# Kernel tuning notes

Measured on AMD Instinct MI355X. Metric: run time of the kernel, lower is better.

The kernel has to match this reference:

```python
import jax, jax.numpy as jnp
import numpy as np

SHIFT, REDUCE = 0, 1
B, T, E, H = 128, 256, 300, 256


def _make_transitions(T, B):
    # Valid left-branching sequence: S, S, (R, S)*, ending with R -> 2T-1 steps.
    t = np.zeros(2 * T - 1, dtype=np.int32)
    t[2::2] = REDUCE
    return np.tile(t[:, None], (1, B))


def setup_inputs() -> dict:
    key = jax.random.key(0)
    ks = jax.random.split(key, 8)
    stdv = 1.0 / np.sqrt(H)
    u = lambda k, shape: jax.random.uniform(k, shape, jnp.float32, -stdv, stdv)
    return {
        "x": jax.random.normal(ks[0], (B, T, E), jnp.float32),
        "transitions": jnp.asarray(_make_transitions(T, B)),
        "Wp": u(ks[1], (E, H)),
        "bp": u(ks[2], (H,)),
        "Wg": u(ks[3], (E, H)),
        "bg": u(ks[4], (H,)),
        "Wr": u(ks[5], (2 * H, 5 * H)),
        "br": u(ks[6], (5 * H,)),
    }


def reference(x, transitions, Wp, bp, Wg, bg, Wr, br):
    Bb, Tt, _ = x.shape
    Hh = Wp.shape[1]
    # buffers: c = proj_x(x); h = sigmoid(proj_x_gate(x)) * tanh(c)
    c_buf = x @ Wp + bp                      # [B, T, H]
    h_buf = jax.nn.sigmoid(x @ Wg + bg) * jnp.tanh(c_buf)
    bidx = jnp.arange(Bb)

    stack_h0 = jnp.zeros((Bb, Tt, Hh), x.dtype)
    stack_c0 = jnp.zeros((Bb, Tt, Hh), x.dtype)
    sp0 = jnp.zeros((Bb,), jnp.int32)        # stack pointer
    bp0 = jnp.full((Bb,), Tt, jnp.int32)     # buffer pointer (pop from end)

    def step(carry, trans):
        sh, sc, sp, bptr = carry
        is_shift = trans == SHIFT            # [B] bool
        # SHIFT: pop last remaining buffer entry
        nbp = jnp.where(is_shift, bptr - 1, bptr)
        src = jnp.maximum(nbp, 0)
        sft_h = h_buf[bidx, src]
        sft_c = c_buf[bidx, src]
        # REDUCE: children = top two stack entries (r = top, l = below)
        ir = jnp.maximum(sp - 1, 0)
        il = jnp.maximum(sp - 2, 0)
        hl, cl = sh[bidx, il], sc[bidx, il]
        hr, cr = sh[bidx, ir], sc[bidx, ir]
        proj = jnp.concatenate([hl, hr], axis=-1) @ Wr + br   # [B, 5H]
        i, fl, fr, g, o = jnp.split(proj, 5, axis=-1)
        c_red = (jax.nn.sigmoid(fl) * cl + jax.nn.sigmoid(fr) * cr
                 + jax.nn.sigmoid(i) * jnp.tanh(g))
        h_red = jax.nn.sigmoid(o) * jnp.tanh(c_red)
        m = is_shift[:, None]
        h_new = jnp.where(m, sft_h, h_red)
        c_new = jnp.where(m, sft_c, c_red)
        pos = jnp.where(is_shift, sp, il)    # push location
        sh = sh.at[bidx, pos].set(h_new)
        sc = sc.at[bidx, pos].set(c_new)
        sp = jnp.where(is_shift, sp + 1, sp - 1)
        return (sh, sc, sp, nbp), None

    (sh, sc, sp, _), _ = jax.lax.scan(step, (stack_h0, stack_c0, sp0, bp0), transitions)
    # root h state = top of stack, h half only
    return sh[bidx, jnp.maximum(sp - 1, 0)]
```

## Files before the change

kernel.cpp:

```cpp
#include <hip/hip_runtime.h>
#include <hip/hip_fp16.h>
#include <math.h>

#define B_ 128
#define T_ 256
#define E_ 300
#define H_ 256
#define N5_ 1280
#define NSTEPS 511
#define DMAX 8

typedef _Float16 half8_t __attribute__((ext_vector_type(8)));
typedef float float4_t __attribute__((ext_vector_type(4)));
typedef unsigned int u4v __attribute__((ext_vector_type(4)));

__device__ __forceinline__ float sigm_p(float x){ return 1.f/(1.f + expf(-x)); }
__device__ __forceinline__ float sigm(float x){ return __builtin_amdgcn_rcpf(1.f + __expf(-x)); }
__device__ __forceinline__ float ftanh(float x){
  float xc = fminf(15.f, fmaxf(-15.f, x));
  float e = __expf(-2.f*xc);
  return (1.f - e) * __builtin_amdgcn_rcpf(1.f + e);
}

__device__ __forceinline__ int dot4(int a, int b, int c){
#if __has_builtin(__builtin_amdgcn_sdot4)
  return __builtin_amdgcn_sdot4(a, b, c, false);
#else
  int d;
  asm("v_dot4_i32_i8 %0, %1, %2, %3" : "=v"(d) : "v"(a), "v"(b), "v"(c));
  return d;
#endif
}

__global__ __launch_bounds__(64) void k0a_scale(const float* __restrict__ Wr,
    float* __restrict__ scales){
  const int n = blockIdx.x, t = threadIdx.x;
  float m = 0.f;
  #pragma unroll
  for (int j=0;j<4;j++) m = fmaxf(m, fabsf(Wr[(size_t)(t+64*j)*N5_ + n]));
  #pragma unroll
  for (int off=32; off; off>>=1) m = fmaxf(m, __shfl_xor(m, off, 64));
  if (t==0) scales[n] = fmaxf(m, 1e-20f) * (1.f/127.f);
}

__global__ __launch_bounds__(256) void k0b_quant(const float* __restrict__ Wr,
    const float* __restrict__ scales, unsigned* __restrict__ W8){
  int idx = blockIdx.x*256 + threadIdx.x;
  if (idx >= 81920) return;
  const int col = idx >> 6, kd = idx & 63;
  const float inv = 1.f / scales[col];
  unsigned acc = 0;
  #pragma unroll
  for (int j=0;j<4;j++){
    float wv = Wr[(size_t)(4*kd + j)*N5_ + col];
    int q = (int)rintf(wv * inv);
    q = q > 127 ? 127 : (q < -127 ? -127 : q);
    acc |= ((unsigned)(q & 255)) << (8*j);
  }
  W8[idx] = acc;
}

__global__ __launch_bounds__(256) void k1_proj(
    const float* __restrict__ x, const float* __restrict__ Wp, const float* __restrict__ bp,
    const float* __restrict__ Wg, const float* __restrict__ bg,
    _Float16* __restrict__ h2, _Float16* __restrict__ c2){
  __shared__ __align__(16) _Float16 As [64*32];
  __shared__ __align__(16) _Float16 BsP[64*32];
  __shared__ __align__(16) _Float16 BsG[64*32];
  const int tid = threadIdx.x;
  const int row0 = blockIdx.x * 64;
  const int n0   = blockIdx.y * 64;
  const int wave = tid >> 6, lane = tid & 63;
  const int ml = lane & 15, quad = lane >> 4;
  float4_t accP[4], accG[4];
  #pragma unroll
  for (int i=0;i<4;i++){ accP[i]=(float4_t)(0.f); accG[i]=(float4_t)(0.f); }
  const int ar = tid >> 2, ak = (tid & 3) * 8;
  const int bk = tid >> 3, bn = (tid & 7) * 8;
  for (int kk = 0; kk < E_; kk += 32){
    __syncthreads();
    {
      const float* src = x + (size_t)(row0 + ar)*E_ + kk + ak;
      float v[8];
      #pragma unroll
      for (int q=0;q<2;q++){
        if (kk + ak + q*4 + 4 <= E_){
          float4_t f = *(const float4_t*)(src + q*4);
          v[q*4+0]=f.x; v[q*4+1]=f.y; v[q*4+2]=f.z; v[q*4+3]=f.w;
        } else {
          #pragma unroll
          for (int j=0;j<4;j++){ int kg = kk+ak+q*4+j; v[q*4+j] = (kg<E_) ? src[q*4+j] : 0.f; }
        }
      }
      #pragma unroll
      for (int j=0;j<8;j++) As[ar*32 + ak + j] = (_Float16)v[j];
    }
    {
      const int kg = kk + bk;
      if (kg < E_){
        const float* sp_ = Wp + (size_t)kg*H_ + n0 + bn;
        const float* sg_ = Wg + (size_t)kg*H_ + n0 + bn;
        float4_t p0 = *(const float4_t*)sp_, p1 = *(const float4_t*)(sp_+4);
        float4_t g0 = *(const float4_t*)sg_, g1 = *(const float4_t*)(sg_+4);
        float pv[8]={p0.x,p0.y,p0.z,p0.w,p1.x,p1.y,p1.z,p1.w};
        float gv[8]={g0.x,g0.y,g0.z,g0.w,g1.x,g1.y,g1.z,g1.w};
        #pragma unroll
        for (int j=0;j<8;j++){ BsP[(bn+j)*32+bk]=(_Float16)pv[j]; BsG[(bn+j)*32+bk]=(_Float16)gv[j]; }
      } else {
        #pragma unroll
        for (int j=0;j<8;j++){ BsP[(bn+j)*32+bk]=(_Float16)0.f; BsG[(bn+j)*32+bk]=(_Float16)0.f; }
      }
    }
    __syncthreads();
    half8_t a = *(const half8_t*)&As[(wave*16 + ml)*32 + quad*8];
    #pragma unroll
    for (int nt=0; nt<4; nt++){
      half8_t b1 = *(const half8_t*)&BsP[(nt*16 + ml)*32 + quad*8];
      accP[nt] = __builtin_amdgcn_mfma_f32_16x16x32_f16(a, b1, accP[nt], 0,0,0);
      half8_t b2 = *(const half8_t*)&BsG[(nt*16 + ml)*32 + quad*8];
      accG[nt] = __builtin_amdgcn_mfma_f32_16x16x32_f16(a, b2, accG[nt], 0,0,0);
    }
  }
  #pragma unroll
  for (int nt=0; nt<4; nt++){
    #pragma unroll
    for (int r=0;r<4;r++){
      int row = row0 + wave*16 + quad*4 + r;
      int col = n0 + nt*16 + ml;
      float c = accP[nt][r] + bp[col];
      float g = accG[nt][r] + bg[col];
      float h = sigm_p(g) * tanhf(c);
      size_t o = (size_t)row*H_ + col;
      c2[o] = (_Float16)c;
      h2[o] = (_Float16)h;
    }
  }
}

__global__ __launch_bounds__(256) void k2_rproj(
    const _Float16* __restrict__ h2, const float* __restrict__ Wr, const float* __restrict__ br,
    _Float16* __restrict__ R2){
  __shared__ __align__(16) _Float16 As[64*32];
  __shared__ __align__(16) _Float16 Bs[64*32];
  const int tid = threadIdx.x;
  const int row0 = blockIdx.x*64, n0 = blockIdx.y*64;
  const int wave = tid>>6, lane = tid&63, ml = lane&15, quad = lane>>4;
  float4_t acc[4];
  #pragma unroll
  for (int i=0;i<4;i++) acc[i]=(float4_t)(0.f);
  const int ar = tid>>2, ak = (tid&3)*8;
  const int bk = tid>>3, bn = (tid&7)*8;
  for (int kk=0; kk<H_; kk+=32){
    __syncthreads();
    *(half8_t*)&As[ar*32+ak] = *(const half8_t*)(h2 + (size_t)(row0+ar)*H_ + kk + ak);
    {
      const float* src = Wr + (size_t)(256 + kk + bk)*N5_ + n0 + bn;
      float4_t f0 = *(const float4_t*)src, f1 = *(const float4_t*)(src+4);
      float v[8]={f0.x,f0.y,f0.z,f0.w,f1.x,f1.y,f1.z,f1.w};
      #pragma unroll
      for (int j=0;j<8;j++) Bs[(bn+j)*32+bk] = (_Float16)v[j];
    }
    __syncthreads();
    half8_t a = *(const half8_t*)&As[(wave*16+ml)*32 + quad*8];
    #pragma unroll
    for (int nt=0; nt<4; nt++){
      half8_t b8 = *(const half8_t*)&Bs[(nt*16+ml)*32 + quad*8];
      acc[nt] = __builtin_amdgcn_mfma_f32_16x16x32_f16(a, b8, acc[nt], 0,0,0);
    }
  }
  #pragma unroll
  for (int nt=0; nt<4; nt++){
    #pragma unroll
    for (int r=0;r<4;r++){
      int row = row0 + wave*16 + quad*4 + r;
      int col = n0 + nt*16 + ml;
      R2[(size_t)row*N5_ + col] = (_Float16)(acc[nt][r] + br[col]);
    }
  }
}

#define BARRIER() asm volatile("s_waitcnt lgkmcnt(0)\n\ts_barrier" ::: "memory")

#define DOT_ALL() \
  _Pragma("unroll") \
  for (int t=0; t<8; t++){ \
    _Pragma("unroll") \
    for (int j=0; j<4; j++){ \
      const int a = (int)aw[t][j]; \
      e0 = dot4(a, (int)wqv[   t][j], e0); \
      e1 = dot4(a, (int)wqv[ 8+t][j], e1); \
      e2 = dot4(a, (int)wqv[16+t][j], e2); \
      e3 = dot4(a, (int)wqv[24+t][j], e3); \
      e4 = dot4(a, (int)wqv[32+t][j], e4); \
    } \
  }

#define COMBINE_HALVES() \
  e0 += __shfl_xor(e0, 32, 64); \
  e1 += __shfl_xor(e1, 32, 64); \
  e2 += __shfl_xor(e2, 32, 64); \
  e3 += __shfl_xor(e3, 32, 64); \
  e4 += __shfl_xor(e4, 32, 64);

#define PAIR_STEP(IDX, RD, WR) { \
  BARRIER(); \
  float a0=(float)pA0, a1=(float)pA1, a2=(float)pA2, a3=(float)pA3, a4=(float)pA4; \
  const float tc = (float)pAc; \
  const u4v* sRD = (const u4v*)(sI8 + (RD)*H_); \
  u4v aw[8]; \
  _Pragma("unroll") \
  for (int t=0; t<8; t++) aw[t] = sRD[hh*8 + t]; \
  { int rrow = 253-(IDX); if (rrow < 0) rrow = 0; \
    const _Float16* rr = R2 + ((size_t)b*T_ + rrow)*N5_ + m; \
    pA0=rr[0]; pA1=rr[256]; pA2=rr[512]; pA3=rr[768]; pA4=rr[1024]; \
    int crow = 252-(IDX); if (crow < 0) crow = 0; \
    pAc = c2[((size_t)b*T_ + crow)*H_ + m]; } \
  int e0=0,e1=0,e2=0,e3=0,e4=0; \
  DOT_ALL() \
  COMBINE_HALVES() \
  a0 += scf0*(float)e0; a1 += scf1*(float)e1; a2 += scf2*(float)e2; \
  a3 += scf3*(float)e3; a4 += scf4*(float)e4; \
  const float cnew = sigm(a1)*cl + sigm(a2)*cr + sigm(a0)*ftanh(a3); \
  const float hnew = sigm(a4)*ftanh(cnew); \
  if (hh == 0) sI8[(WR)*H_ + m] = (char)(int)rintf(hnew*127.f); \
  cl = cnew; cr = tc; \
}

__global__ __launch_bounds__(512, 2) void k3_scan(
    const int* __restrict__ trans, const _Float16* __restrict__ h2, const _Float16* __restrict__ c2,
    const _Float16* __restrict__ R2, const unsigned* __restrict__ W8,
    const float* __restrict__ scales, const float* __restrict__ Wr,
    const float* __restrict__ br, float* __restrict__ out){
  __shared__ float sh_[DMAX*H_];
  __shared__ float sc_[DMAX*H_];
  __shared__ __align__(16) char sI8[DMAX*H_];
  __shared__ int trs[NSTEPS+1];

  const int b = blockIdx.x, tid = threadIdx.x;
  const int lane = tid & 63, w8 = tid >> 6;
  const int m  = w8*32 + (lane & 31);
  const int hh = (lane >> 5) & 1;

  u4v wqv[40];
  #pragma unroll
  for (int g=0; g<5; g++){
    const u4v* src = (const u4v*)(W8 + (size_t)(g*256 + m)*64 + hh*32);
    #pragma unroll
    for (int t=0; t<8; t++) wqv[g*8 + t] = src[t];
  }

  const float scf0 = scales[m       ] * (1.f/127.f);
  const float scf1 = scales[m +  256] * (1.f/127.f);
  const float scf2 = scales[m +  512] * (1.f/127.f);
  const float scf3 = scales[m +  768] * (1.f/127.f);
  const float scf4 = scales[m + 1024] * (1.f/127.f);

  trs[tid] = (tid < NSTEPS) ? trans[(size_t)tid*B_ + b] : 1;
  for (int i = tid; i < DMAX*H_; i += 512){ sh_[i]=0.f; sc_[i]=0.f; sI8[i]=0; }

  int myok = 1;
  if (tid < NSTEPS){ int e = (tid>=2 && (tid&1)==0) ? 1 : 0; if (trs[tid]!=e) myok=0; }
  const int ok = __syncthreads_and(myok);

  if (ok){
    const size_t hb = (size_t)b*T_*H_;
    const _Float16 h255 = h2[hb + 255*H_ + m];
    float cl = (float)c2[hb + 255*H_ + m];
    float cr = (float)c2[hb + 254*H_ + m];
    _Float16 pA0,pA1,pA2,pA3,pA4,pAc;
    { const _Float16* rr = R2 + ((size_t)b*T_ + 254)*N5_ + m;
      pA0=rr[0]; pA1=rr[256]; pA2=rr[512]; pA3=rr[768]; pA4=rr[1024];
      pAc = c2[hb + 253*H_ + m]; }
    if (hh == 0) sI8[m] = (char)(int)rintf((float)h255 * 127.f);
    #pragma unroll 1
    for (int i=0; i<254; i+=2){
      PAIR_STEP(i,   0, 1)
      PAIR_STEP(i+1, 1, 0)
    }
    {
      BARRIER();
      float a0=(float)pA0, a1=(float)pA1, a2=(float)pA2, a3=(float)pA3, a4=(float)pA4;
      const u4v* sRD = (const u4v*)sI8;
      u4v aw[8];
      #pragma unroll
      for (int t=0; t<8; t++) aw[t] = sRD[hh*8 + t];
      int e0=0,e1=0,e2=0,e3=0,e4=0;
      DOT_ALL()
      COMBINE_HALVES()
      a0 += scf0*(float)e0; a1 += scf1*(float)e1; a2 += scf2*(float)e2;
      a3 += scf3*(float)e3; a4 += scf4*(float)e4;
      const float cnew = sigm(a1)*cl + sigm(a2)*cr + sigm(a0)*ftanh(a3);
      const float hnew = sigm(a4)*ftanh(cnew);
      if (hh == 0) out[(size_t)b*H_ + m] = hnew;
    }
    return;
  }

  int sp = 0, bptr = T_, prev_src = -1;
  for (int step=0; step<NSTEPS; step++){
    __syncthreads();
    const int tr = trs[step];
    if (tr == 0){
      const int nbp = bptr - 1;
      const int src = nbp > 0 ? nbp : 0;
      const int slot = sp < 0 ? 0 : (sp > DMAX-1 ? DMAX-1 : sp);
      const size_t o = ((size_t)b*T_ + src)*H_ + m;
      const float wh = (float)h2[o], wc = (float)c2[o];
      if (hh == 0){
        sh_[slot*H_+m] = wh;
        sc_[slot*H_+m] = wc;
        sI8[slot*H_+m] = (char)(int)rintf(wh * 127.f);
      }
      sp += 1; bptr = nbp; prev_src = src;
    } else {
      int ir = sp-1 > 0 ? sp-1 : 0;
      int il = sp-2 > 0 ? sp-2 : 0;
      ir = ir > DMAX-1 ? DMAX-1 : ir;
      il = il > DMAX-1 ? DMAX-1 : il;
      const int tg = prev_src;
      const float cl = sc_[il*H_+m];
      const float cr = sc_[ir*H_+m];
      const u4v* sRD = (const u4v*)(sI8 + il*H_);
      u4v aw[8];
      #pragma unroll
      for (int t=0; t<8; t++) aw[t] = sRD[hh*8 + t];
      float a0,a1,a2,a3,a4;
      if (tg >= 0){
        const _Float16* rr = R2 + ((size_t)b*T_ + tg)*N5_ + m;
        a0=(float)rr[0]; a1=(float)rr[256]; a2=(float)rr[512]; a3=(float)rr[768]; a4=(float)rr[1024];
      } else {
        a0=br[m]; a1=br[m+256]; a2=br[m+512]; a3=br[m+768]; a4=br[m+1024];
      }
      int e0=0,e1=0,e2=0,e3=0,e4=0;
      DOT_ALL()
      COMBINE_HALVES()
      a0 += scf0*(float)e0; a1 += scf1*(float)e1; a2 += scf2*(float)e2;
      a3 += scf3*(float)e3; a4 += scf4*(float)e4;
      if (tg < 0){
        for (int k=0; k<H_; k++){
          const float hrk = sh_[ir*H_+k];
          const float* wr = Wr + (size_t)(256+k)*N5_ + m;
          a0 += hrk*wr[0]; a1 += hrk*wr[256]; a2 += hrk*wr[512];
          a3 += hrk*wr[768]; a4 += hrk*wr[1024];
        }
      }
      const float cnew = sigm(a1)*cl + sigm(a2)*cr + sigm(a0)*ftanh(a3);
      const float hnew = sigm(a4)*ftanh(cnew);
      const int wq = (int)rintf(hnew * 127.f);
      __syncthreads();
      if (hh == 0){
        sh_[il*H_+m] = hnew;
        sc_[il*H_+m] = cnew;
        sI8[il*H_+m] = (char)wq;
      }
      sp -= 1; prev_src = -1;
    }
  }
  __syncthreads();
  int fs = sp-1 > 0 ? sp-1 : 0;
  fs = fs > DMAX-1 ? DMAX-1 : fs;
  if (hh == 0) out[(size_t)b*H_ + m] = sh_[fs*H_+m];
}

extern "C" void kernel_launch(void* const* d_in, const int* in_sizes, int n_in,
                              void* d_out, int out_size, void* d_ws, size_t ws_size,
                              hipStream_t stream){
  const float* x    = (const float*)d_in[0];
  const int*   trn  = (const int*)  d_in[1];
  const float* Wp   = (const float*)d_in[2];
  const float* bp   = (const float*)d_in[3];
  const float* Wg   = (const float*)d_in[4];
  const float* bg   = (const float*)d_in[5];
  const float* Wr   = (const float*)d_in[6];
  const float* br   = (const float*)d_in[7];
  float* out = (float*)d_out;
  char* w = (char*)d_ws;
  _Float16* h2   = (_Float16*)(w);
  _Float16* c2   = (_Float16*)(w + (size_t)16777216);
  _Float16* R2   = (_Float16*)(w + (size_t)33554432);
  unsigned* W8   = (unsigned*)(w + (size_t)117440512);
  float*    scl  = (float*)   (w + (size_t)117768192);

  hipLaunchKernelGGL(k0a_scale, dim3(1280),    dim3(64),  0, stream, Wr, scl);
  hipLaunchKernelGGL(k0b_quant, dim3(320),     dim3(256), 0, stream, Wr, scl, W8);
  hipLaunchKernelGGL(k1_proj,   dim3(512, 4),  dim3(256), 0, stream, x, Wp, bp, Wg, bg, h2, c2);
  hipLaunchKernelGGL(k2_rproj,  dim3(512, 20), dim3(256), 0, stream, h2, Wr, br, R2);
  hipLaunchKernelGGL(k3_scan,   dim3(128),     dim3(512), 0, stream, trn, h2, c2, R2, W8, scl, Wr, br, out);
}
```

Measured before the change: 543.6 us.

## Move three gate matvecs in scan to int8 MFMA with AGPR-resident weights

In the recurrent scan, three of the five gate projections move from per-lane v_dot4 loops to v_mfma_i32_16x16x64_i8 chains. The weights for these are repacked into MFMA B-fragment layout by a new quantization kernel and kept in AGPRs. The remaining two gates keep dot4 and now reduce halves with permlane32_swap. The goal is to shorten the serial per-step compute latency and ease VGPR pressure. The cost is explicit s_nop fencing, an extra prep kernel, and wasted MFMA columns, since the matvec has only one useful row.

```diff
diff --git a/kernel.cpp b/kernel.cpp
--- a/kernel.cpp
+++ b/kernel.cpp
@@ -12,6 +12,7 @@
 
 typedef _Float16 half8_t __attribute__((ext_vector_type(8)));
 typedef float float4_t __attribute__((ext_vector_type(4)));
+typedef int i4v __attribute__((ext_vector_type(4)));
 typedef unsigned int u4v __attribute__((ext_vector_type(4)));
 
 __device__ __forceinline__ float sigm_p(float x){ return 1.f/(1.f + expf(-x)); }
@@ -32,6 +33,16 @@
 #endif
 }
 
+__device__ __forceinline__ int sum_halves(int e){
+#if __has_builtin(__builtin_amdgcn_permlane32_swap)
+  typedef unsigned u2v __attribute__((ext_vector_type(2)));
+  u2v r = __builtin_amdgcn_permlane32_swap((unsigned)e, (unsigned)e, false, false);
+  return (int)r[0] + (int)r[1];
+#else
+  return e + __shfl_xor(e, 32, 64);
+#endif
+}
+
 __global__ __launch_bounds__(64) void k0a_scale(const float* __restrict__ Wr,
     float* __restrict__ scales){
   const int n = blockIdx.x, t = threadIdx.x;
@@ -58,6 +69,38 @@
     acc |= ((unsigned)(q & 255)) << (8*j);
   }
   W8[idx] = acc;
+}
+
+__global__ __launch_bounds__(256) void k0c_quant(const float* __restrict__ Wr,
+    const float* __restrict__ scales, uint4* __restrict__ W4){
+  int idx = blockIdx.x*256 + threadIdx.x;
+  if (idx >= 20480) return;
+  const int f    = idx >> 6;
+  const int lane = idx & 63;
+  const int w    = f / 80;
+  const int r80  = f - w*80;
+  const int g    = r80 >> 4;
+  const int cg   = (r80 >> 2) & 3;
+  const int kc   = r80 & 3;
+  const int ml   = lane & 15, quad = lane >> 4;
+  const int col  = g*256 + w*64 + cg*16 + ml;
+  const float inv = 1.f / scales[col];
+  unsigned int d[4];
+  #pragma unroll
+  for (int r=0; r<4; r++){
+    unsigned int acc = 0;
+    #pragma unroll
+    for (int j=0; j<4; j++){
+      const int k = kc*64 + quad*16 + r*4 + j;
+      float wv = Wr[(size_t)k*N5_ + col];
+      int q = (int)rintf(wv * inv);
+      q = q > 127 ? 127 : (q < -127 ? -127 : q);
+      acc |= ((unsigned int)(q & 255)) << (8*j);
+    }
+    d[r] = acc;
+  }
+  uint4 v; v.x=d[0]; v.y=d[1]; v.z=d[2]; v.w=d[3];
+  W4[idx] = v;
 }
 
 __global__ __launch_bounds__(256) void k1_proj(
@@ -181,32 +224,46 @@
 
 #define BARRIER() asm volatile("s_waitcnt lgkmcnt(0)\n\ts_barrier" ::: "memory")
 
-#define DOT_ALL() \
+#define DECL8(g) u4v bf##g##_0_0, bf##g##_0_1, bf##g##_0_2, bf##g##_0_3, \
+                     bf##g##_1_0, bf##g##_1_1, bf##g##_1_2, bf##g##_1_3;
+#define LOAD8(g) \
+  bf##g##_0_0 = wb[((g)*16 + 0)*64]; bf##g##_0_1 = wb[((g)*16 + 1)*64]; \
+  bf##g##_0_2 = wb[((g)*16 + 2)*64]; bf##g##_0_3 = wb[((g)*16 + 3)*64]; \
+  bf##g##_1_0 = wb[((g)*16 + 4)*64]; bf##g##_1_1 = wb[((g)*16 + 5)*64]; \
+  bf##g##_1_2 = wb[((g)*16 + 6)*64]; bf##g##_1_3 = wb[((g)*16 + 7)*64];
+
+#define MFA(ACC, AF, BF) asm("v_mfma_i32_16x16x64_i8 %0, %1, %2, %0" \
+    : "+v"(ACC) : "v"(AF), "a"(BF));
+#define FENCE_IN2(A0,A1)  asm volatile("s_nop 1" : "+v"(A0), "+v"(A1));
+#define FENCE_OUT2(A0,A1) asm volatile("s_nop 7\n\ts_nop 7" : "+v"(A0), "+v"(A1));
+
+#define GCHAIN2(g, DST) { \
+  i4v A0={0,0,0,0}, A1={0,0,0,0}; \
+  FENCE_IN2(A0,A1) \
+  MFA(A0,af0,bf##g##_0_0) MFA(A1,af0,bf##g##_1_0) \
+  MFA(A0,af1,bf##g##_0_1) MFA(A1,af1,bf##g##_1_1) \
+  MFA(A0,af2,bf##g##_0_2) MFA(A1,af2,bf##g##_1_2) \
+  MFA(A0,af3,bf##g##_0_3) MFA(A1,af3,bf##g##_1_3) \
+  FENCE_OUT2(A0,A1) \
+  DST = hsel ? A1.x : A0.x; }
+
+#define DOT2() \
   _Pragma("unroll") \
   for (int t=0; t<8; t++){ \
     _Pragma("unroll") \
     for (int j=0; j<4; j++){ \
       const int a = (int)aw[t][j]; \
-      e0 = dot4(a, (int)wqv[   t][j], e0); \
-      e1 = dot4(a, (int)wqv[ 8+t][j], e1); \
-      e2 = dot4(a, (int)wqv[16+t][j], e2); \
-      e3 = dot4(a, (int)wqv[24+t][j], e3); \
-      e4 = dot4(a, (int)wqv[32+t][j], e4); \
+      e3 = dot4(a, (int)wq3[t][j], e3); \
+      e4 = dot4(a, (int)wq4[t][j], e4); \
     } \
   }
-
-#define COMBINE_HALVES() \
-  e0 += __shfl_xor(e0, 32, 64); \
-  e1 += __shfl_xor(e1, 32, 64); \
-  e2 += __shfl_xor(e2, 32, 64); \
-  e3 += __shfl_xor(e3, 32, 64); \
-  e4 += __shfl_xor(e4, 32, 64);
 
 #define PAIR_STEP(IDX, RD, WR) { \
   BARRIER(); \
   float a0=(float)pA0, a1=(float)pA1, a2=(float)pA2, a3=(float)pA3, a4=(float)pA4; \
   const float tc = (float)pAc; \
   const u4v* sRD = (const u4v*)(sI8 + (RD)*H_); \
+  const u4v af0 = sRD[quad], af1 = sRD[4+quad], af2 = sRD[8+quad], af3 = sRD[12+quad]; \
   u4v aw[8]; \
   _Pragma("unroll") \
   for (int t=0; t<8; t++) aw[t] = sRD[hh*8 + t]; \
@@ -215,10 +272,14 @@
     pA0=rr[0]; pA1=rr[256]; pA2=rr[512]; pA3=rr[768]; pA4=rr[1024]; \
     int crow = 252-(IDX); if (crow < 0) crow = 0; \
     pAc = c2[((size_t)b*T_ + crow)*H_ + m]; } \
-  int e0=0,e1=0,e2=0,e3=0,e4=0; \
-  DOT_ALL() \
-  COMBINE_HALVES() \
-  a0 += scf0*(float)e0; a1 += scf1*(float)e1; a2 += scf2*(float)e2; \
+  int e3=0, e4=0; \
+  DOT2() \
+  int d0,d1,d2; \
+  GCHAIN2(0, d0) \
+  GCHAIN2(1, d1) \
+  GCHAIN2(2, d2) \
+  e3 = sum_halves(e3); e4 = sum_halves(e4); \
+  a0 += scf0*(float)d0; a1 += scf1*(float)d1; a2 += scf2*(float)d2; \
   a3 += scf3*(float)e3; a4 += scf4*(float)e4; \
   const float cnew = sigm(a1)*cl + sigm(a2)*cr + sigm(a0)*ftanh(a3); \
   const float hnew = sigm(a4)*ftanh(cnew); \
@@ -228,25 +289,36 @@
 
 __global__ __launch_bounds__(512, 2) void k3_scan(
     const int* __restrict__ trans, const _Float16* __restrict__ h2, const _Float16* __restrict__ c2,
-    const _Float16* __restrict__ R2, const unsigned* __restrict__ W8,
+    const _Float16* __restrict__ R2, const uint4* __restrict__ W4,
+    const unsigned* __restrict__ W8,
     const float* __restrict__ scales, const float* __restrict__ Wr,
     const float* __restrict__ br, float* __restrict__ out){
   __shared__ float sh_[DMAX*H_];
   __shared__ float sc_[DMAX*H_];
   __shared__ __align__(16) char sI8[DMAX*H_];
   __shared__ int trs[NSTEPS+1];
+  const u4v* sI4 = (const u4v*)sI8;
 
   const int b = blockIdx.x, tid = threadIdx.x;
   const int lane = tid & 63, w8 = tid >> 6;
-  const int m  = w8*32 + (lane & 31);
-  const int hh = (lane >> 5) & 1;
-
-  u4v wqv[40];
-  #pragma unroll
-  for (int g=0; g<5; g++){
-    const u4v* src = (const u4v*)(W8 + (size_t)(g*256 + m)*64 + hh*32);
-    #pragma unroll
-    for (int t=0; t<8; t++) wqv[g*8 + t] = src[t];
+  const int quad = (lane >> 4) & 3;
+  const int hsel = (lane >> 4) & 1;
+  const int hh   = (lane >> 5) & 1;
+  const int m    = (w8 << 5) + (lane & 31);
+  const int w4   = w8 >> 1, cg0 = (w8 & 1) * 2;
+
+  const u4v* WB4v = (const u4v*)W4;
+  const u4v* wb   = WB4v + ((size_t)w4*80 + cg0*4)*64 + lane;
+
+  DECL8(0) DECL8(1) DECL8(2)
+  LOAD8(0) LOAD8(1) LOAD8(2)
+
+  u4v wq3[8], wq4[8];
+  {
+    const u4v* s3 = (const u4v*)(W8 + (size_t)(3*256 + m)*64 + hh*32);
+    const u4v* s4 = (const u4v*)(W8 + (size_t)(4*256 + m)*64 + hh*32);
+    #pragma unroll
+    for (int t=0;t<8;t++){ wq3[t]=s3[t]; wq4[t]=s4[t]; }
   }
 
   const float scf0 = scales[m       ] * (1.f/127.f);
@@ -281,13 +353,18 @@
       BARRIER();
       float a0=(float)pA0, a1=(float)pA1, a2=(float)pA2, a3=(float)pA3, a4=(float)pA4;
       const u4v* sRD = (const u4v*)sI8;
+      const u4v af0 = sRD[quad], af1 = sRD[4+quad], af2 = sRD[8+quad], af3 = sRD[12+quad];
       u4v aw[8];
       #pragma unroll
       for (int t=0; t<8; t++) aw[t] = sRD[hh*8 + t];
-      int e0=0,e1=0,e2=0,e3=0,e4=0;
-      DOT_ALL()
-      COMBINE_HALVES()
-      a0 += scf0*(float)e0; a1 += scf1*(float)e1; a2 += scf2*(float)e2;
+      int e3=0, e4=0;
+      DOT2()
+      int d0,d1,d2;
+      GCHAIN2(0, d0)
+      GCHAIN2(1, d1)
+      GCHAIN2(2, d2)
+      e3 = sum_halves(e3); e4 = sum_halves(e4);
+      a0 += scf0*(float)d0; a1 += scf1*(float)d1; a2 += scf2*(float)d2;
       a3 += scf3*(float)e3; a4 += scf4*(float)e4;
       const float cnew = sigm(a1)*cl + sigm(a2)*cr + sigm(a0)*ftanh(a3);
       const float hnew = sigm(a4)*ftanh(cnew);
@@ -320,10 +397,13 @@
       const int tg = prev_src;
       const float cl = sc_[il*H_+m];
       const float cr = sc_[ir*H_+m];
-      const u4v* sRD = (const u4v*)(sI8 + il*H_);
+      const u4v af0 = sI4[il*16 +  0 + quad];
+      const u4v af1 = sI4[il*16 +  4 + quad];
+      const u4v af2 = sI4[il*16 +  8 + quad];
+      const u4v af3 = sI4[il*16 + 12 + quad];
       u4v aw[8];
       #pragma unroll
-      for (int t=0; t<8; t++) aw[t] = sRD[hh*8 + t];
+      for (int t=0; t<8; t++) aw[t] = ((const u4v*)(sI8 + il*H_))[hh*8 + t];
       float a0,a1,a2,a3,a4;
       if (tg >= 0){
         const _Float16* rr = R2 + ((size_t)b*T_ + tg)*N5_ + m;
@@ -331,10 +411,14 @@
       } else {
         a0=br[m]; a1=br[m+256]; a2=br[m+512]; a3=br[m+768]; a4=br[m+1024];
       }
-      int e0=0,e1=0,e2=0,e3=0,e4=0;
-      DOT_ALL()
-      COMBINE_HALVES()
-      a0 += scf0*(float)e0; a1 += scf1*(float)e1; a2 += scf2*(float)e2;
+      int e3=0, e4=0;
+      DOT2()
+      int d0,d1,d2;
+      GCHAIN2(0, d0)
+      GCHAIN2(1, d1)
+      GCHAIN2(2, d2)
+      e3 = sum_halves(e3); e4 = sum_halves(e4);
+      a0 += scf0*(float)d0; a1 += scf1*(float)d1; a2 += scf2*(float)d2;
       a3 += scf3*(float)e3; a4 += scf4*(float)e4;
       if (tg < 0){
         for (int k=0; k<H_; k++){
@@ -378,12 +462,14 @@
   _Float16* h2   = (_Float16*)(w);
   _Float16* c2   = (_Float16*)(w + (size_t)16777216);
   _Float16* R2   = (_Float16*)(w + (size_t)33554432);
-  unsigned* W8   = (unsigned*)(w + (size_t)117440512);
+  uint4*    W4   = (uint4*)   (w + (size_t)117440512);
   float*    scl  = (float*)   (w + (size_t)117768192);
+  unsigned* W8   = (unsigned*)(w + (size_t)117773312);
 
   hipLaunchKernelGGL(k0a_scale, dim3(1280),    dim3(64),  0, stream, Wr, scl);
   hipLaunchKernelGGL(k0b_quant, dim3(320),     dim3(256), 0, stream, Wr, scl, W8);
+  hipLaunchKernelGGL(k0c_quant, dim3(80),      dim3(256), 0, stream, Wr, scl, W4);
   hipLaunchKernelGGL(k1_proj,   dim3(512, 4),  dim3(256), 0, stream, x, Wp, bp, Wg, bg, h2, c2);
   hipLaunchKernelGGL(k2_rproj,  dim3(512, 20), dim3(256), 0, stream, h2, Wr, br, R2);
-  hipLaunchKernelGGL(k3_scan,   dim3(128),     dim3(512), 0, stream, trn, h2, c2, R2, W8, scl, Wr, br, out);
-}
+  hipLaunchKernelGGL(k3_scan,   dim3(128),     dim3(512), 0, stream, trn, h2, c2, R2, W4, W8, scl, Wr, br, out);
+}
```

Measured after the change: 591.7 us. 1.09x slower.
